# Kernel optimization log

Measured on AMD Instinct MI355X. Metric: run time of the kernel, lower is better.

Reference implementation:

```python
import jax, jax.numpy as jnp
import numpy as np

DIM = 128
HEADS = 8
HEAD_DIM = DIM // HEADS
K = 5          # kernel_size per spatial axis
DIL = 1        # dilation
EPS = 1e-5


def setup_inputs() -> dict:
    key = jax.random.key(0)
    ks = jax.random.split(key, 12)
    s = 0.02
    inp = {
        "x": jax.random.normal(ks[0], (1, DIM, 16, 16, 4), jnp.float32),
        "skip": jax.random.normal(ks[1], (1, DIM, 32, 32, 8), jnp.float32),
        "Wq": jax.random.normal(ks[2], (DIM, DIM), jnp.float32) * s,
        "bq": jnp.zeros((DIM,), jnp.float32),
        "Wk": jax.random.normal(ks[3], (DIM, DIM), jnp.float32) * s,
        "bk": jnp.zeros((DIM,), jnp.float32),
        "Wv": jax.random.normal(ks[4], (DIM, DIM), jnp.float32) * s,
        "bv": jnp.zeros((DIM,), jnp.float32),
        "rpb": jax.random.normal(ks[5], (HEADS, 2 * K - 1, 2 * K - 1, 2 * K - 1), jnp.float32) * s,
        "Wo": jax.random.normal(ks[6], (DIM, DIM), jnp.float32) * s,
        "bo": jnp.zeros((DIM,), jnp.float32),
    }
    return inp


def _instance_norm(t):
    # InstanceNorm3d, affine=False: normalize over spatial dims per (B, C)
    mu = jnp.mean(t, axis=(2, 3, 4), keepdims=True)
    var = jnp.var(t, axis=(2, 3, 4), keepdims=True)
    return (t - mu) * jax.lax.rsqrt(var + EPS)


def _nbr_idx(L):
    # NATTEN-style clamped window: start shifted to stay in bounds
    i = np.arange(L)
    start = np.clip(i - (K // 2) * DIL, 0, L - 1 - (K - 1) * DIL)
    idx = start[:, None] + np.arange(K)[None, :] * DIL  # (L, K)
    rel = (idx - i[:, None]) // DIL + (K - 1)           # (L, K) in [0, 2K-2]
    return jnp.asarray(idx), jnp.asarray(rel)


def reference(x, skip, Wq, bq, Wk, bk, Wv, bv, rpb, Wo, bo):
    x = _instance_norm(x)
    skip = _instance_norm(skip)

    xu = jnp.repeat(jnp.repeat(jnp.repeat(x, 2, axis=2), 2, axis=3), 2, axis=4)

    B, C, H, W, Z = skip.shape
    N = H * W * Z
    xt = xu.transpose(0, 2, 3, 4, 1).reshape(B, N, C)    # queries from upsampled x
    st = skip.transpose(0, 2, 3, 4, 1).reshape(B, N, C)  # keys/values from skip

    def heads(t):
        return t.reshape(B, N, HEADS, HEAD_DIM).transpose(0, 2, 1, 3)  # (B,h,N,d)

    q = heads(xt @ Wq + bq) * (HEAD_DIM ** -0.5)
    k = heads(st @ Wk + bk)
    v = heads(st @ Wv + bv)

    idxH, relH = _nbr_idx(H)
    idxW, relW = _nbr_idx(W)
    idxZ, relZ = _nbr_idx(Z)

    # flattened neighbor token indices: (N, K^3)
    nbr = (idxH[:, None, None, :, None, None] * (W * Z)
           + idxW[None, :, None, None, :, None] * Z
           + idxZ[None, None, :, None, None, :])
    nbr = jnp.broadcast_to(nbr, (H, W, Z, K, K, K)).reshape(N, K ** 3)

    # relative position bias gather: (heads, N, K^3)
    rH = jnp.broadcast_to(relH[:, None, None, :, None, None], (H, W, Z, K, K, K)).reshape(N, K ** 3)
    rW = jnp.broadcast_to(relW[None, :, None, None, :, None], (H, W, Z, K, K, K)).reshape(N, K ** 3)
    rZ = jnp.broadcast_to(relZ[None, None, :, None, None, :], (H, W, Z, K, K, K)).reshape(N, K ** 3)
    bias = rpb[:, rH, rW, rZ]  # (heads, N, K^3)

    kg = jnp.take(k, nbr, axis=2)  # (B, h, N, K^3, d)
    vg = jnp.take(v, nbr, axis=2)

    logits = jnp.einsum('bhnd,bhnkd->bhnk', q, kg) + bias[None]
    attn = jax.nn.softmax(logits, axis=-1)
    out = jnp.einsum('bhnk,bhnkd->bhnd', attn, vg)

    out = out.transpose(0, 2, 1, 3).reshape(B, N, C) @ Wo + bo
    return out.reshape(B, H, W, Z, C).transpose(0, 4, 1, 2, 3)
```

## Files before the change

### kernel.cpp

```cpp
#include <hip/hip_runtime.h>
#include <math.h>

#define DIM 128
#define HEADS 8
#define HD 16
#define NPOS 8192
#define EPS 1e-5f

static __device__ __forceinline__ unsigned short f2bf(float f) {
    unsigned u = __float_as_uint(f);
    return (unsigned short)((u + 0x7fffu + ((u >> 16) & 1u)) >> 16);
}
#define BLO(u) __uint_as_float((u) << 16)
#define BHI(u) __uint_as_float((u) & 0xffff0000u)

__global__ __launch_bounds__(256) void stats_kernel(const float* __restrict__ x,
                                                    const float* __restrict__ skip,
                                                    float* __restrict__ ws) {
    int c = blockIdx.x;
    const float* src; int n; float* mu_out; float* rs_out; int ci;
    if (c < DIM) { ci = c; src = x + c * 1024; n = 1024; mu_out = ws; rs_out = ws + DIM; }
    else { ci = c - DIM; src = skip + (size_t)ci * NPOS; n = NPOS; mu_out = ws + 2*DIM; rs_out = ws + 3*DIM; }
    int t = threadIdx.x;
    float s = 0.f, s2 = 0.f;
    for (int i = t; i < n; i += 256) { float v = src[i]; s += v; s2 = fmaf(v, v, s2); }
    #pragma unroll
    for (int off = 32; off > 0; off >>= 1) {
        s  += __shfl_down(s,  off, 64);
        s2 += __shfl_down(s2, off, 64);
    }
    __shared__ float ls[4], ls2[4];
    int wv = t >> 6;
    if ((t & 63) == 0) { ls[wv] = s; ls2[wv] = s2; }
    __syncthreads();
    if (t == 0) {
        float S  = ls[0] + ls[1] + ls[2] + ls[3];
        float S2 = ls2[0] + ls2[1] + ls2[2] + ls2[3];
        float inv_n = 1.f / (float)n;
        float mu  = S * inv_n;
        float var = S2 * inv_n - mu * mu;
        mu_out[ci] = mu;
        rs_out[ci] = rsqrtf(var + EPS);
    }
}

__global__ __launch_bounds__(512) void prep_kernel(const float* __restrict__ Wq, const float* __restrict__ bq,
                                                   const float* __restrict__ Wk, const float* __restrict__ bk,
                                                   const float* __restrict__ Wv, const float* __restrict__ bv,
                                                   const float* __restrict__ ws,
                                                   float* __restrict__ Wp, float* __restrict__ bp) {
    int m = blockIdx.x;
    const float* W = (m == 0) ? Wq : (m == 1) ? Wk : Wv;
    const float* b = (m == 0) ? bq : (m == 1) ? bk : bv;
    const float* mu = (m == 0) ? ws : ws + 2*DIM;
    const float* rs = (m == 0) ? ws + DIM : ws + 3*DIM;
    float scale = (m == 0) ? 0.25f : 1.0f;

    int t = threadIdx.x;
    int j = blockIdx.y * 32 + (t & 31);
    int g = t >> 5;
    float acc = 0.f;
    for (int ci = g * 8; ci < g * 8 + 8; ++ci) {
        float w  = W[ci * 128 + j];
        float wp = rs[ci] * w * scale;
        Wp[m * 16384 + ci * 128 + j] = wp;
        acc = fmaf(mu[ci], wp, acc);
    }
    __shared__ float red[512];
    red[t] = acc;
    __syncthreads();
    if (g == 0) {
        float ssum = 0.f;
        #pragma unroll
        for (int r = 0; r < 16; ++r) ssum += red[r * 32 + (t & 31)];
        bp[m * 128 + j] = scale * b[j] - ssum;
    }
}

__global__ __launch_bounds__(256) void qkv_kernel(const float* __restrict__ x,
                                                  const float* __restrict__ skip,
                                                  const float* __restrict__ Wp,
                                                  const float* __restrict__ bp,
                                                  float* __restrict__ q_out,
                                                  float* __restrict__ k_out,
                                                  float* __restrict__ v_out) {
    __shared__ float at[128 * 68];
    __shared__ float wl[128 * 64];
    int t = threadIdx.x;
    int which = blockIdx.y;
    int half  = blockIdx.z;
    int n0 = blockIdx.x * 64;

    {
        const float4* W4 = (const float4*)(Wp + which * 16384);
        float4* wl4 = (float4*)wl;
        for (int i4 = t; i4 < 2048; i4 += 256) {
            int ci = i4 >> 4, j4 = i4 & 15;
            wl4[ci * 16 + j4] = W4[ci * 32 + half * 16 + j4];
        }
    }
    if (which == 0) {
        for (int i4 = t; i4 < 2048; i4 += 256) {
            int ci = i4 >> 4, ln4 = (i4 & 15) * 4;
            int n = n0 + ln4;
            int hc = n >> 8, wc = (n >> 3) & 31, zc = n & 7;
            float2 f = *(const float2*)(x + ci * 1024 + (hc >> 1) * 64 + (wc >> 1) * 4 + (zc >> 1));
            *(float4*)(at + ci * 68 + ln4) = make_float4(f.x, f.x, f.y, f.y);
        }
    } else {
        for (int i4 = t; i4 < 2048; i4 += 256) {
            int ci = i4 >> 4, ln4 = (i4 & 15) * 4;
            float4 f = *(const float4*)(skip + (size_t)ci * NPOS + n0 + ln4);
            *(float4*)(at + ci * 68 + ln4) = f;
        }
    }
    __syncthreads();

    int pg = t & 15, cg = t >> 4;
    const float* bb = bp + which * 128 + half * 64 + cg * 4;
    float4 bv4 = *(const float4*)bb;
    float4 acc[4];
    #pragma unroll
    for (int ps = 0; ps < 4; ++ps) acc[ps] = bv4;

    const float* ap = at + pg * 4;
    const float* wp = wl + cg * 4;
    #pragma unroll 4
    for (int ci = 0; ci < 128; ++ci) {
        float4 a4 = *(const float4*)(ap + ci * 68);
        float4 w4 = *(const float4*)(wp + ci * 64);
        float av[4] = { a4.x, a4.y, a4.z, a4.w };
        #pragma unroll
        for (int ps = 0; ps < 4; ++ps) {
            float a = av[ps];
            acc[ps].x = fmaf(a, w4.x, acc[ps].x);
            acc[ps].y = fmaf(a, w4.y, acc[ps].y);
            acc[ps].z = fmaf(a, w4.z, acc[ps].z);
            acc[ps].w = fmaf(a, w4.w, acc[ps].w);
        }
    }
    float* outp = (which == 0) ? q_out : (which == 1) ? k_out : v_out;
    int p0 = n0 + pg * 4;
    #pragma unroll
    for (int ps = 0; ps < 4; ++ps)
        *(float4*)(outp + (size_t)(p0 + ps) * 128 + half * 64 + cg * 4) = acc[ps];
}

__global__ __launch_bounds__(512) void attn_kernel(const float* __restrict__ q,
                                                   const float* __restrict__ k,
                                                   const float* __restrict__ v,
                                                   const float* __restrict__ rpb,
                                                   float* __restrict__ ao_t) {
    __shared__ __align__(16) unsigned short kbf[2 * 520 * 8];
    __shared__ __align__(16) unsigned short vbf[2 * 520 * 8];
    __shared__ float bias_l[729];

    int blk = blockIdx.x;
    int h    = blk & 7;
    int tile = blk >> 3;
    int h0 = (tile >> 3) * 4;
    int w0 = (tile & 7) * 4;
    int bh0 = min(max(h0 - 2, 0), 24);
    int bw0 = min(max(w0 - 2, 0), 24);
    int t = threadIdx.x;

    for (int idx = t; idx < 1024; idx += 512) {
        int nbr = idx >> 1, c2 = idx & 1;
        int nh = nbr >> 6, nw = (nbr >> 3) & 7, nz = nbr & 7;
        int n = (bh0 + nh) * 256 + (bw0 + nw) * 8 + nz;
        int base = nh * 64 + nz * 8 + ((nw + nz) & 7);
        const float* kp = k + (size_t)n * 128 + h * 16 + c2 * 8;
        const float* vp = v + (size_t)n * 128 + h * 16 + c2 * 8;
        float4 ka = *(const float4*)kp;
        float4 kb = *(const float4*)(kp + 4);
        float4 va = *(const float4*)vp;
        float4 vb = *(const float4*)(vp + 4);
        uint4 pk, pv;
        pk.x = ((unsigned)f2bf(ka.y) << 16) | f2bf(ka.x);
        pk.y = ((unsigned)f2bf(ka.w) << 16) | f2bf(ka.z);
        pk.z = ((unsigned)f2bf(kb.y) << 16) | f2bf(kb.x);
        pk.w = ((unsigned)f2bf(kb.w) << 16) | f2bf(kb.z);
        pv.x = ((unsigned)f2bf(va.y) << 16) | f2bf(va.x);
        pv.y = ((unsigned)f2bf(va.w) << 16) | f2bf(va.z);
        pv.z = ((unsigned)f2bf(vb.y) << 16) | f2bf(vb.x);
        pv.w = ((unsigned)f2bf(vb.w) << 16) | f2bf(vb.z);
        *(uint4*)(kbf + (c2 * 520 + base) * 8) = pk;
        *(uint4*)(vbf + (c2 * 520 + base) * 8) = pv;
    }
    for (int idx = t; idx < 729; idx += 512) bias_l[idx] = rpb[h * 729 + idx];
    __syncthreads();

    int s = t & 3, p = t >> 2;
    int ph = p >> 5, pw = (p >> 3) & 3, pz = p & 7;
    int hc = h0 + ph, wc = w0 + pw, zc = pz;
    int sh = min(max(hc - 2, 0), 27);
    int sw = min(max(wc - 2, 0), 27);
    int sz = min(max(zc - 2, 0), 3);
    int hb = sh - bh0, wb = sw - bw0;
    int bias_base = (sh - hc + 4) * 81 + (sw - wc + 4) * 9 + (sz - zc + 4);
    int n = hc * 256 + wc * 8 + zc;

    float qv[16];
    #pragma unroll
    for (int i = 0; i < 4; ++i)
        ((float4*)qv)[i] = *(const float4*)(q + (size_t)n * 128 + h * 16 + i * 4);

    float o[16];
    #pragma unroll
    for (int d = 0; d < 16; ++d) o[d] = 0.f;
    float l = 0.f;

    int cnt   = s ? 31 : 32;
    int start = s * 31 + (s ? 1 : 0);
    int i0 = p & 31; if (i0 >= cnt) i0 -= cnt;

    for (int it = 0; it < cnt; ++it) {
        int ii = i0 + it; if (ii >= cnt) ii -= cnt;
        int j = start + ii;
        int jh = (j * 41) >> 10;
        int jr = j - jh * 25;
        int jw = (jr * 13) >> 6;
        int jz = jr - jw * 5;
        int nz = sz + jz;
        int base = (hb + jh) * 64 + nz * 8 + ((wb + jw + nz) & 7);
        float bias = bias_l[bias_base + jh * 81 + jw * 9 + jz];

        uint4 ka = *(const uint4*)(kbf + base * 8);
        uint4 kb = *(const uint4*)(kbf + (520 + base) * 8);
        float d0 = 0.f, d1 = 0.f, d2 = 0.f, d3 = 0.f;
        d0 = fmaf(BLO(ka.x), qv[0],  d0);
        d0 = fmaf(BHI(ka.x), qv[1],  d0);
        d0 = fmaf(BLO(ka.y), qv[2],  d0);
        d0 = fmaf(BHI(ka.y), qv[3],  d0);
        d1 = fmaf(BLO(ka.z), qv[4],  d1);
        d1 = fmaf(BHI(ka.z), qv[5],  d1);
        d1 = fmaf(BLO(ka.w), qv[6],  d1);
        d1 = fmaf(BHI(ka.w), qv[7],  d1);
        d2 = fmaf(BLO(kb.x), qv[8],  d2);
        d2 = fmaf(BHI(kb.x), qv[9],  d2);
        d2 = fmaf(BLO(kb.y), qv[10], d2);
        d2 = fmaf(BHI(kb.y), qv[11], d2);
        d3 = fmaf(BLO(kb.z), qv[12], d3);
        d3 = fmaf(BHI(kb.z), qv[13], d3);
        d3 = fmaf(BLO(kb.w), qv[14], d3);
        d3 = fmaf(BHI(kb.w), qv[15], d3);
        float sc = (d0 + d1) + (d2 + d3) + bias;
        float pp = __expf(sc);
        l += pp;

        uint4 va = *(const uint4*)(vbf + base * 8);
        uint4 vb = *(const uint4*)(vbf + (520 + base) * 8);
        o[0]  = fmaf(pp, BLO(va.x), o[0]);
        o[1]  = fmaf(pp, BHI(va.x), o[1]);
        o[2]  = fmaf(pp, BLO(va.y), o[2]);
        o[3]  = fmaf(pp, BHI(va.y), o[3]);
        o[4]  = fmaf(pp, BLO(va.z), o[4]);
        o[5]  = fmaf(pp, BHI(va.z), o[5]);
        o[6]  = fmaf(pp, BLO(va.w), o[6]);
        o[7]  = fmaf(pp, BHI(va.w), o[7]);
        o[8]  = fmaf(pp, BLO(vb.x), o[8]);
        o[9]  = fmaf(pp, BHI(vb.x), o[9]);
        o[10] = fmaf(pp, BLO(vb.y), o[10]);
        o[11] = fmaf(pp, BHI(vb.y), o[11]);
        o[12] = fmaf(pp, BLO(vb.z), o[12]);
        o[13] = fmaf(pp, BHI(vb.z), o[13]);
        o[14] = fmaf(pp, BLO(vb.w), o[14]);
        o[15] = fmaf(pp, BHI(vb.w), o[15]);
    }

    #pragma unroll
    for (int step = 1; step <= 2; step <<= 1) {
        l += __shfl_xor(l, step, 64);
        #pragma unroll
        for (int d = 0; d < 16; ++d) o[d] += __shfl_xor(o[d], step, 64);
    }
    float inv = 1.f / l;
    #pragma unroll
    for (int j = 0; j < 4; ++j)
        ao_t[(size_t)(h * 16 + s * 4 + j) * NPOS + n] = o[4 * s + j] * inv;
}

__global__ __launch_bounds__(256) void proj_kernel(const float* __restrict__ ao_t,
                                                   const float* __restrict__ Wo,
                                                   const float* __restrict__ bo,
                                                   float* __restrict__ out) {
    __shared__ float at[128 * 68];
    __shared__ float wl[128 * 64];
    int t = threadIdx.x;
    int half = blockIdx.y;
    int n0 = blockIdx.x * 64;

    {
        const float4* W4 = (const float4*)Wo;
        float4* wl4 = (float4*)wl;
        for (int i4 = t; i4 < 2048; i4 += 256) {
            int ci = i4 >> 4, j4 = i4 & 15;
            wl4[ci * 16 + j4] = W4[ci * 32 + half * 16 + j4];
        }
    }
    for (int i4 = t; i4 < 2048; i4 += 256) {
        int ci = i4 >> 4, ln4 = (i4 & 15) * 4;
        float4 f = *(const float4*)(ao_t + (size_t)ci * NPOS + n0 + ln4);
        *(float4*)(at + ci * 68 + ln4) = f;
    }
    __syncthreads();

    int pg = t & 15, cg = t >> 4;
    float4 bv4 = *(const float4*)(bo + half * 64 + cg * 4);
    float4 acc[4];
    #pragma unroll
    for (int ps = 0; ps < 4; ++ps) acc[ps] = bv4;

    const float* ap = at + pg * 4;
    const float* wp = wl + cg * 4;
    #pragma unroll 4
    for (int ci = 0; ci < 128; ++ci) {
        float4 a4 = *(const float4*)(ap + ci * 68);
        float4 w4 = *(const float4*)(wp + ci * 64);
        float av[4] = { a4.x, a4.y, a4.z, a4.w };
        #pragma unroll
        for (int ps = 0; ps < 4; ++ps) {
            float a = av[ps];
            acc[ps].x = fmaf(a, w4.x, acc[ps].x);
            acc[ps].y = fmaf(a, w4.y, acc[ps].y);
            acc[ps].z = fmaf(a, w4.z, acc[ps].z);
            acc[ps].w = fmaf(a, w4.w, acc[ps].w);
        }
    }
    int p0 = n0 + pg * 4;
    int jbase = half * 64 + cg * 4;
    *(float4*)(out + (size_t)(jbase + 0) * NPOS + p0) = make_float4(acc[0].x, acc[1].x, acc[2].x, acc[3].x);
    *(float4*)(out + (size_t)(jbase + 1) * NPOS + p0) = make_float4(acc[0].y, acc[1].y, acc[2].y, acc[3].y);
    *(float4*)(out + (size_t)(jbase + 2) * NPOS + p0) = make_float4(acc[0].z, acc[1].z, acc[2].z, acc[3].z);
    *(float4*)(out + (size_t)(jbase + 3) * NPOS + p0) = make_float4(acc[0].w, acc[1].w, acc[2].w, acc[3].w);
}

extern "C" void kernel_launch(void* const* d_in, const int* in_sizes, int n_in,
                              void* d_out, int out_size, void* d_ws, size_t ws_size,
                              hipStream_t stream) {
    const float* x    = (const float*)d_in[0];
    const float* skip = (const float*)d_in[1];
    const float* Wq   = (const float*)d_in[2];
    const float* bq   = (const float*)d_in[3];
    const float* Wk   = (const float*)d_in[4];
    const float* bk   = (const float*)d_in[5];
    const float* Wv   = (const float*)d_in[6];
    const float* bv   = (const float*)d_in[7];
    const float* rpb  = (const float*)d_in[8];
    const float* Wo   = (const float*)d_in[9];
    const float* bo   = (const float*)d_in[10];
    float* out = (float*)d_out;

    float* ws   = (float*)d_ws;
    float* q    = ws  + 512;
    float* k    = q   + (size_t)NPOS * 128;
    float* v    = k   + (size_t)NPOS * 128;
    float* ao_t = v   + (size_t)NPOS * 128;
    float* Wp   = ao_t + (size_t)NPOS * 128;
    float* bp   = Wp  + 3 * 16384;

    stats_kernel<<<256, 256, 0, stream>>>(x, skip, ws);
    prep_kernel<<<dim3(3, 4), 512, 0, stream>>>(Wq, bq, Wk, bk, Wv, bv, ws, Wp, bp);
    qkv_kernel<<<dim3(128, 3, 2), 256, 0, stream>>>(x, skip, Wp, bp, q, k, v);
    attn_kernel<<<512, 512, 0, stream>>>(q, k, v, rpb, ao_t);
    proj_kernel<<<dim3(128, 2), 256, 0, stream>>>(ao_t, Wo, bo, out);
}
```

Baseline: 144.1 us.

## Fuse norm into QKV, emit bf16 K/V, split attention tiles finer

Removes the prep kernel and applies instance-norm mean/rstd directly when staging activations in the QKV GEMM, with the q scale applied at the store. K and V are written as packed bf16 from the QKV kernel, which halves their global traffic and removes the conversion step from attention. The attention kernel now uses half-width tiles (1024 blocks), 8 threads per query instead of 4, and smaller shared halos with a launch-bounds occupancy hint. The trade is more halo reloading per block and an extra shuffle reduction step.

```diff
diff --git a/kernel.cpp b/kernel.cpp
--- a/kernel.cpp
+++ b/kernel.cpp
@@ -44,46 +44,15 @@
     }
 }
 
-__global__ __launch_bounds__(512) void prep_kernel(const float* __restrict__ Wq, const float* __restrict__ bq,
-                                                   const float* __restrict__ Wk, const float* __restrict__ bk,
-                                                   const float* __restrict__ Wv, const float* __restrict__ bv,
-                                                   const float* __restrict__ ws,
-                                                   float* __restrict__ Wp, float* __restrict__ bp) {
-    int m = blockIdx.x;
-    const float* W = (m == 0) ? Wq : (m == 1) ? Wk : Wv;
-    const float* b = (m == 0) ? bq : (m == 1) ? bk : bv;
-    const float* mu = (m == 0) ? ws : ws + 2*DIM;
-    const float* rs = (m == 0) ? ws + DIM : ws + 3*DIM;
-    float scale = (m == 0) ? 0.25f : 1.0f;
-
-    int t = threadIdx.x;
-    int j = blockIdx.y * 32 + (t & 31);
-    int g = t >> 5;
-    float acc = 0.f;
-    for (int ci = g * 8; ci < g * 8 + 8; ++ci) {
-        float w  = W[ci * 128 + j];
-        float wp = rs[ci] * w * scale;
-        Wp[m * 16384 + ci * 128 + j] = wp;
-        acc = fmaf(mu[ci], wp, acc);
-    }
-    __shared__ float red[512];
-    red[t] = acc;
-    __syncthreads();
-    if (g == 0) {
-        float ssum = 0.f;
-        #pragma unroll
-        for (int r = 0; r < 16; ++r) ssum += red[r * 32 + (t & 31)];
-        bp[m * 128 + j] = scale * b[j] - ssum;
-    }
-}
-
 __global__ __launch_bounds__(256) void qkv_kernel(const float* __restrict__ x,
                                                   const float* __restrict__ skip,
-                                                  const float* __restrict__ Wp,
-                                                  const float* __restrict__ bp,
+                                                  const float* __restrict__ Wq, const float* __restrict__ bq,
+                                                  const float* __restrict__ Wk, const float* __restrict__ bk,
+                                                  const float* __restrict__ Wv, const float* __restrict__ bv,
+                                                  const float* __restrict__ ws,
                                                   float* __restrict__ q_out,
-                                                  float* __restrict__ k_out,
-                                                  float* __restrict__ v_out) {
+                                                  unsigned* __restrict__ k_out,
+                                                  unsigned* __restrict__ v_out) {
     __shared__ float at[128 * 68];
     __shared__ float wl[128 * 64];
     int t = threadIdx.x;
@@ -91,34 +60,41 @@
     int half  = blockIdx.z;
     int n0 = blockIdx.x * 64;
 
+    const float* W = (which == 0) ? Wq : (which == 1) ? Wk : Wv;
+    const float* b = (which == 0) ? bq : (which == 1) ? bk : bv;
     {
-        const float4* W4 = (const float4*)(Wp + which * 16384);
+        const float4* W4 = (const float4*)W;
         float4* wl4 = (float4*)wl;
         for (int i4 = t; i4 < 2048; i4 += 256) {
             int ci = i4 >> 4, j4 = i4 & 15;
             wl4[ci * 16 + j4] = W4[ci * 32 + half * 16 + j4];
         }
     }
+    const float* mu = (which == 0) ? ws : ws + 2*DIM;
+    const float* rs = (which == 0) ? ws + DIM : ws + 3*DIM;
     if (which == 0) {
         for (int i4 = t; i4 < 2048; i4 += 256) {
             int ci = i4 >> 4, ln4 = (i4 & 15) * 4;
             int n = n0 + ln4;
             int hc = n >> 8, wc = (n >> 3) & 31, zc = n & 7;
             float2 f = *(const float2*)(x + ci * 1024 + (hc >> 1) * 64 + (wc >> 1) * 4 + (zc >> 1));
-            *(float4*)(at + ci * 68 + ln4) = make_float4(f.x, f.x, f.y, f.y);
+            float m_ = mu[ci], r_ = rs[ci];
+            float a0 = (f.x - m_) * r_, a1 = (f.y - m_) * r_;
+            *(float4*)(at + ci * 68 + ln4) = make_float4(a0, a0, a1, a1);
         }
     } else {
         for (int i4 = t; i4 < 2048; i4 += 256) {
             int ci = i4 >> 4, ln4 = (i4 & 15) * 4;
             float4 f = *(const float4*)(skip + (size_t)ci * NPOS + n0 + ln4);
-            *(float4*)(at + ci * 68 + ln4) = f;
+            float m_ = mu[ci], r_ = rs[ci];
+            *(float4*)(at + ci * 68 + ln4) =
+                make_float4((f.x - m_) * r_, (f.y - m_) * r_, (f.z - m_) * r_, (f.w - m_) * r_);
         }
     }
     __syncthreads();
 
     int pg = t & 15, cg = t >> 4;
-    const float* bb = bp + which * 128 + half * 64 + cg * 4;
-    float4 bv4 = *(const float4*)bb;
+    float4 bv4 = *(const float4*)(b + half * 64 + cg * 4);
     float4 acc[4];
     #pragma unroll
     for (int ps = 0; ps < 4; ++ps) acc[ps] = bv4;
@@ -139,59 +115,63 @@
             acc[ps].w = fmaf(a, w4.w, acc[ps].w);
         }
     }
-    float* outp = (which == 0) ? q_out : (which == 1) ? k_out : v_out;
     int p0 = n0 + pg * 4;
-    #pragma unroll
-    for (int ps = 0; ps < 4; ++ps)
-        *(float4*)(outp + (size_t)(p0 + ps) * 128 + half * 64 + cg * 4) = acc[ps];
-}
-
-__global__ __launch_bounds__(512) void attn_kernel(const float* __restrict__ q,
-                                                   const float* __restrict__ k,
-                                                   const float* __restrict__ v,
-                                                   const float* __restrict__ rpb,
-                                                   float* __restrict__ ao_t) {
-    __shared__ __align__(16) unsigned short kbf[2 * 520 * 8];
-    __shared__ __align__(16) unsigned short vbf[2 * 520 * 8];
+    if (which == 0) {
+        #pragma unroll
+        for (int ps = 0; ps < 4; ++ps) {
+            float4 r = make_float4(acc[ps].x * 0.25f, acc[ps].y * 0.25f,
+                                   acc[ps].z * 0.25f, acc[ps].w * 0.25f);
+            *(float4*)(q_out + (size_t)(p0 + ps) * 128 + half * 64 + cg * 4) = r;
+        }
+    } else {
+        unsigned* outp = (which == 1) ? k_out : v_out;
+        #pragma unroll
+        for (int ps = 0; ps < 4; ++ps) {
+            uint2 pk;
+            pk.x = ((unsigned)f2bf(acc[ps].y) << 16) | f2bf(acc[ps].x);
+            pk.y = ((unsigned)f2bf(acc[ps].w) << 16) | f2bf(acc[ps].z);
+            *(uint2*)(outp + (size_t)(p0 + ps) * 64 + half * 32 + cg * 2) = pk;
+        }
+    }
+}
+
+__global__ __launch_bounds__(512, 6) void attn_kernel(const float* __restrict__ q,
+                                                      const unsigned* __restrict__ kb,
+                                                      const unsigned* __restrict__ vb,
+                                                      const float* __restrict__ rpb,
+                                                      float* __restrict__ ao_t) {
+    __shared__ uint4 kbf[2 * 416];
+    __shared__ uint4 vbf[2 * 416];
     __shared__ float bias_l[729];
 
     int blk = blockIdx.x;
-    int h    = blk & 7;
-    int tile = blk >> 3;
+    int h     = blk & 7;
+    int rest  = blk >> 3;
+    int halfw = rest & 1;
+    int tile  = rest >> 1;
     int h0 = (tile >> 3) * 4;
-    int w0 = (tile & 7) * 4;
+    int w0 = (tile & 7) * 4 + halfw * 2;
     int bh0 = min(max(h0 - 2, 0), 24);
-    int bw0 = min(max(w0 - 2, 0), 24);
+    int bw0 = min(max(w0 - 2, 0), 26);
     int t = threadIdx.x;
 
-    for (int idx = t; idx < 1024; idx += 512) {
-        int nbr = idx >> 1, c2 = idx & 1;
-        int nh = nbr >> 6, nw = (nbr >> 3) & 7, nz = nbr & 7;
+    for (int idx = t; idx < 768; idx += 512) {
+        int c2 = idx & 1;
+        int r  = idx >> 1;
+        int nz = r & 7;
+        int q2 = r >> 3;
+        int nh = (q2 * 43) >> 8;
+        int nw = q2 - nh * 6;
         int n = (bh0 + nh) * 256 + (bw0 + nw) * 8 + nz;
-        int base = nh * 64 + nz * 8 + ((nw + nz) & 7);
-        const float* kp = k + (size_t)n * 128 + h * 16 + c2 * 8;
-        const float* vp = v + (size_t)n * 128 + h * 16 + c2 * 8;
-        float4 ka = *(const float4*)kp;
-        float4 kb = *(const float4*)(kp + 4);
-        float4 va = *(const float4*)vp;
-        float4 vb = *(const float4*)(vp + 4);
-        uint4 pk, pv;
-        pk.x = ((unsigned)f2bf(ka.y) << 16) | f2bf(ka.x);
-        pk.y = ((unsigned)f2bf(ka.w) << 16) | f2bf(ka.z);
-        pk.z = ((unsigned)f2bf(kb.y) << 16) | f2bf(kb.x);
-        pk.w = ((unsigned)f2bf(kb.w) << 16) | f2bf(kb.z);
-        pv.x = ((unsigned)f2bf(va.y) << 16) | f2bf(va.x);
-        pv.y = ((unsigned)f2bf(va.w) << 16) | f2bf(va.z);
-        pv.z = ((unsigned)f2bf(vb.y) << 16) | f2bf(vb.x);
-        pv.w = ((unsigned)f2bf(vb.w) << 16) | f2bf(vb.z);
-        *(uint4*)(kbf + (c2 * 520 + base) * 8) = pk;
-        *(uint4*)(vbf + (c2 * 520 + base) * 8) = pv;
+        int base = nh * 52 + nw * 8 + ((nz + nw) & 7);
+        kbf[c2 * 416 + base] = *(const uint4*)(kb + (size_t)n * 64 + h * 8 + c2 * 4);
+        vbf[c2 * 416 + base] = *(const uint4*)(vb + (size_t)n * 64 + h * 8 + c2 * 4);
     }
     for (int idx = t; idx < 729; idx += 512) bias_l[idx] = rpb[h * 729 + idx];
     __syncthreads();
 
-    int s = t & 3, p = t >> 2;
-    int ph = p >> 5, pw = (p >> 3) & 3, pz = p & 7;
+    int s = t & 7, p = t >> 3;
+    int ph = p >> 4, pw = (p >> 3) & 1, pz = p & 7;
     int hc = h0 + ph, wc = w0 + pw, zc = pz;
     int sh = min(max(hc - 2, 0), 27);
     int sw = min(max(wc - 2, 0), 27);
@@ -210,9 +190,9 @@
     for (int d = 0; d < 16; ++d) o[d] = 0.f;
     float l = 0.f;
 
-    int cnt   = s ? 31 : 32;
-    int start = s * 31 + (s ? 1 : 0);
-    int i0 = p & 31; if (i0 >= cnt) i0 -= cnt;
+    int cnt   = (s < 5) ? 16 : 15;
+    int start = (s < 5) ? 16 * s : 15 * s + 5;
+    int i0 = p & 15; if (i0 >= cnt) i0 -= cnt;
 
     for (int it = 0; it < cnt; ++it) {
         int ii = i0 + it; if (ii >= cnt) ii -= cnt;
@@ -221,12 +201,13 @@
         int jr = j - jh * 25;
         int jw = (jr * 13) >> 6;
         int jz = jr - jw * 5;
-        int nz = sz + jz;
-        int base = (hb + jh) * 64 + nz * 8 + ((wb + jw + nz) & 7);
+        int nnw = wb + jw;
+        int nnz = sz + jz;
+        int base = (hb + jh) * 52 + nnw * 8 + ((nnz + nnw) & 7);
         float bias = bias_l[bias_base + jh * 81 + jw * 9 + jz];
 
-        uint4 ka = *(const uint4*)(kbf + base * 8);
-        uint4 kb = *(const uint4*)(kbf + (520 + base) * 8);
+        uint4 ka = kbf[base];
+        uint4 k2 = kbf[416 + base];
         float d0 = 0.f, d1 = 0.f, d2 = 0.f, d3 = 0.f;
         d0 = fmaf(BLO(ka.x), qv[0],  d0);
         d0 = fmaf(BHI(ka.x), qv[1],  d0);
@@ -236,20 +217,20 @@
         d1 = fmaf(BHI(ka.z), qv[5],  d1);
         d1 = fmaf(BLO(ka.w), qv[6],  d1);
         d1 = fmaf(BHI(ka.w), qv[7],  d1);
-        d2 = fmaf(BLO(kb.x), qv[8],  d2);
-        d2 = fmaf(BHI(kb.x), qv[9],  d2);
-        d2 = fmaf(BLO(kb.y), qv[10], d2);
-        d2 = fmaf(BHI(kb.y), qv[11], d2);
-        d3 = fmaf(BLO(kb.z), qv[12], d3);
-        d3 = fmaf(BHI(kb.z), qv[13], d3);
-        d3 = fmaf(BLO(kb.w), qv[14], d3);
-        d3 = fmaf(BHI(kb.w), qv[15], d3);
+        d2 = fmaf(BLO(k2.x), qv[8],  d2);
+        d2 = fmaf(BHI(k2.x), qv[9],  d2);
+        d2 = fmaf(BLO(k2.y), qv[10], d2);
+        d2 = fmaf(BHI(k2.y), qv[11], d2);
+        d3 = fmaf(BLO(k2.z), qv[12], d3);
+        d3 = fmaf(BHI(k2.z), qv[13], d3);
+        d3 = fmaf(BLO(k2.w), qv[14], d3);
+        d3 = fmaf(BHI(k2.w), qv[15], d3);
         float sc = (d0 + d1) + (d2 + d3) + bias;
         float pp = __expf(sc);
         l += pp;
 
-        uint4 va = *(const uint4*)(vbf + base * 8);
-        uint4 vb = *(const uint4*)(vbf + (520 + base) * 8);
+        uint4 va = vbf[base];
+        uint4 v2 = vbf[416 + base];
         o[0]  = fmaf(pp, BLO(va.x), o[0]);
         o[1]  = fmaf(pp, BHI(va.x), o[1]);
         o[2]  = fmaf(pp, BLO(va.y), o[2]);
@@ -258,26 +239,25 @@
         o[5]  = fmaf(pp, BHI(va.z), o[5]);
         o[6]  = fmaf(pp, BLO(va.w), o[6]);
         o[7]  = fmaf(pp, BHI(va.w), o[7]);
-        o[8]  = fmaf(pp, BLO(vb.x), o[8]);
-        o[9]  = fmaf(pp, BHI(vb.x), o[9]);
-        o[10] = fmaf(pp, BLO(vb.y), o[10]);
-        o[11] = fmaf(pp, BHI(vb.y), o[11]);
-        o[12] = fmaf(pp, BLO(vb.z), o[12]);
-        o[13] = fmaf(pp, BHI(vb.z), o[13]);
-        o[14] = fmaf(pp, BLO(vb.w), o[14]);
-        o[15] = fmaf(pp, BHI(vb.w), o[15]);
-    }
-
-    #pragma unroll
-    for (int step = 1; step <= 2; step <<= 1) {
+        o[8]  = fmaf(pp, BLO(v2.x), o[8]);
+        o[9]  = fmaf(pp, BHI(v2.x), o[9]);
+        o[10] = fmaf(pp, BLO(v2.y), o[10]);
+        o[11] = fmaf(pp, BHI(v2.y), o[11]);
+        o[12] = fmaf(pp, BLO(v2.z), o[12]);
+        o[13] = fmaf(pp, BHI(v2.z), o[13]);
+        o[14] = fmaf(pp, BLO(v2.w), o[14]);
+        o[15] = fmaf(pp, BHI(v2.w), o[15]);
+    }
+
+    #pragma unroll
+    for (int step = 1; step <= 4; step <<= 1) {
         l += __shfl_xor(l, step, 64);
         #pragma unroll
         for (int d = 0; d < 16; ++d) o[d] += __shfl_xor(o[d], step, 64);
     }
     float inv = 1.f / l;
-    #pragma unroll
-    for (int j = 0; j < 4; ++j)
-        ao_t[(size_t)(h * 16 + s * 4 + j) * NPOS + n] = o[4 * s + j] * inv;
+    ao_t[(size_t)(h * 16 + 2 * s)     * NPOS + n] = o[2 * s]     * inv;
+    ao_t[(size_t)(h * 16 + 2 * s + 1) * NPOS + n] = o[2 * s + 1] * inv;
 }
 
 __global__ __launch_bounds__(256) void proj_kernel(const float* __restrict__ ao_t,
@@ -351,17 +331,14 @@
     const float* bo   = (const float*)d_in[10];
     float* out = (float*)d_out;
 
-    float* ws   = (float*)d_ws;
-    float* q    = ws  + 512;
-    float* k    = q   + (size_t)NPOS * 128;
-    float* v    = k   + (size_t)NPOS * 128;
-    float* ao_t = v   + (size_t)NPOS * 128;
-    float* Wp   = ao_t + (size_t)NPOS * 128;
-    float* bp   = Wp  + 3 * 16384;
+    float*    ws   = (float*)d_ws;
+    float*    q    = ws + 512;
+    unsigned* kbp  = (unsigned*)(q + (size_t)NPOS * 128);
+    unsigned* vbp  = kbp + (size_t)NPOS * 64;
+    float*    ao_t = (float*)(vbp + (size_t)NPOS * 64);
 
     stats_kernel<<<256, 256, 0, stream>>>(x, skip, ws);
-    prep_kernel<<<dim3(3, 4), 512, 0, stream>>>(Wq, bq, Wk, bk, Wv, bv, ws, Wp, bp);
-    qkv_kernel<<<dim3(128, 3, 2), 256, 0, stream>>>(x, skip, Wp, bp, q, k, v);
-    attn_kernel<<<512, 512, 0, stream>>>(q, k, v, rpb, ao_t);
+    qkv_kernel<<<dim3(128, 3, 2), 256, 0, stream>>>(x, skip, Wq, bq, Wk, bk, Wv, bv, ws, q, kbp, vbp);
+    attn_kernel<<<1024, 512, 0, stream>>>(q, kbp, vbp, rpb, ao_t);
     proj_kernel<<<dim3(128, 2), 256, 0, stream>>>(ao_t, Wo, bo, out);
 }
```

Measured after the change: 142.4 us. Within noise of the previous version (-1.2%).
